# Kernel optimization log

Measured on AMD Instinct MI355X. Metric: run time of the kernel, lower is better.

The kernel has to match this reference:

```python
import jax, jax.numpy as jnp
import numpy as np

WS = 800      # window size
HEADS = 3
DH = 24       # dim_head
LOWRANK_W = 30
NEG_SLOPE = 0.01  # LeakyReLU default
LN_EPS = 1e-5


def _layernorm(x, g, b):
    m = jnp.mean(x, axis=-1, keepdims=True)
    v = jnp.var(x, axis=-1, keepdims=True)
    return (x - m) * jax.lax.rsqrt(v + LN_EPS) * g + b


def setup_inputs() -> dict:
    key = jax.random.key(0)
    ks = jax.random.split(key, 20)
    B, CIN, H, W = 2, 5, 160, 160
    D = 48
    INNER = HEADS * DH  # 72
    f32 = jnp.float32

    def n(k, shape, s=0.05):
        return jax.random.normal(k, shape, f32) * s

    return {
        "x": jax.random.normal(ks[0], (B, CIN, H, W), f32),
        # Embedding: Conv2d(5, 48, 3, pad=1) + PReLU
        "conv_w": n(ks[1], (D, CIN, 3, 3), 0.1),
        "conv_b": jnp.zeros((D,), f32),
        "prelu_a": jnp.array(0.25, f32),
        # attention PreNorm
        "ln1_g": jnp.ones((D,), f32),
        "ln1_b": jnp.zeros((D,), f32),
        # to_qkv: Linear(48, 216, bias=False)
        "w_qkv": n(ks[2], (3 * INNER, D)),
        # Linformer low-rank params E,F: [heads, dim_head, w]
        "E_mat": jax.random.normal(ks[3], (HEADS, DH, LOWRANK_W), f32),
        "F_mat": jax.random.normal(ks[4], (HEADS, DH, LOWRANK_W), f32),
        # lin1/lin2: Linear(w, dim_head)
        "w_e": n(ks[5], (DH, LOWRANK_W)),
        "b_e": jnp.zeros((DH,), f32),
        "w_f": n(ks[6], (DH, LOWRANK_W)),
        "b_f": jnp.zeros((DH,), f32),
        # to_out: Linear(72, 48)
        "w_out": n(ks[7], (D, INNER)),
        "b_out": jnp.zeros((D,), f32),
        # FF PreNorm + MLP (dim=48, hidden=48)
        "ln2_g": jnp.ones((D,), f32),
        "ln2_b": jnp.zeros((D,), f32),
        "ff_w1": n(ks[8], (D, D)),
        "ff_b1": jnp.zeros((D,), f32),
        "ff_w2": n(ks[9], (D, D)),
        "ff_b2": jnp.zeros((D,), f32),
        # final lin1: Linear(48, 96)
        "w_fin": n(ks[10], (2 * D, D)),
        "b_fin": jnp.zeros((2 * D,), f32),
    }


def reference(x, conv_w, conv_b, prelu_a, ln1_g, ln1_b, w_qkv, E_mat, F_mat,
              w_e, b_e, w_f, b_f, w_out, b_out, ln2_g, ln2_b,
              ff_w1, ff_b1, ff_w2, ff_b2, w_fin, b_fin):
    B, _, H, W = x.shape
    # Embedding: conv3x3 same + PReLU
    E = jax.lax.conv_general_dilated(
        x, conv_w, (1, 1), ((1, 1), (1, 1)),
        dimension_numbers=("NCHW", "OIHW", "NCHW")) + conv_b[None, :, None, None]
    E = jnp.maximum(E, 0) + prelu_a * jnp.minimum(E, 0)
    D = E.shape[1]
    seq = E.reshape(B, D, H * W).transpose(0, 2, 1)  # [B, N, D]
    N = seq.shape[1]
    nw = N // WS

    # --- Residual(PreNorm(LinformerAttention_wind1)) ---
    xn = _layernorm(seq, ln1_g, ln1_b)
    xw = xn.reshape(B, nw, WS, D)                         # windows
    qkv = jnp.einsum("bwnc,oc->bwno", xw, w_qkv)          # [B,nw,WS,216]
    qkv = qkv.reshape(B, nw, WS, HEADS, 3 * DH).transpose(0, 1, 3, 2, 4)
    q, k, v = jnp.split(qkv, 3, axis=-1)                  # each [B,nw,h,WS,DH]
    # einsum 'b h n d, h d d -> b h n d' == scale by diagonal of lin(E/F)
    e_diag = jnp.einsum("hdw,dw->hd", E_mat, w_e) + b_e   # [h, DH]
    f_diag = jnp.einsum("hdw,dw->hd", F_mat, w_f) + b_f
    k = k * e_diag[None, None, :, None, :]
    v = v * f_diag[None, None, :, None, :]
    scale = DH ** -0.5
    dots = jnp.einsum("bwhid,bwhjd->bwhij", q, k) * scale  # [B,nw,h,WS,WS]
    attn = jax.nn.softmax(dots, axis=-1)
    ow = jnp.einsum("bwhij,bwhjd->bwhid", attn, v)
    ow = ow.transpose(0, 1, 3, 2, 4).reshape(B, N, HEADS * DH)
    att = jnp.einsum("bnf,of->bno", ow, w_out) + b_out
    seq = seq + att

    # --- Residual(PreNorm(FeedForward)) ---
    yn = _layernorm(seq, ln2_g, ln2_b)
    h = jnp.einsum("bnc,oc->bno", yn, ff_w1) + ff_b1
    h = jnp.where(h >= 0, h, NEG_SLOPE * h)
    h = jnp.einsum("bno,co->bnc", h, ff_w2) + ff_b2
    att1 = seq + h                                        # [B, N, D]

    hp = att1.transpose(0, 2, 1).reshape(B, D, H, W)
    Highpass1 = E * hp + E
    lin = jnp.einsum("bnc,oc->bno", att1, w_fin) + b_fin  # [B, N, 2D]
    return (Highpass1, lin)
```

## Files before the change

kernel.cpp:

```cpp
#include <hip/hip_runtime.h>
#include <hip/hip_bf16.h>

#define B_    2
#define CIN_  5
#define H_    160
#define W_    160
#define N_    25600
#define D_    48
#define NW_   32
#define WS_   800
#define HEADS_ 3
#define DH_   24
#define INNER_ 72
#define NWH_  192

typedef __bf16 bf16x8 __attribute__((ext_vector_type(8)));
typedef float  f32x4  __attribute__((ext_vector_type(4)));

#define MFMA(a,b,c) __builtin_amdgcn_mfma_f32_16x16x32_bf16((a),(b),(c),0,0,0)

__device__ __forceinline__ float fast_exp2(float x) {
#if __has_builtin(__builtin_amdgcn_exp2f)
    return __builtin_amdgcn_exp2f(x);
#else
    return exp2f(x);
#endif
}

__device__ __forceinline__ unsigned pack_bf16(float lo, float hi) {
    __bf16 l = (__bf16)lo, h = (__bf16)hi;
    unsigned short ul = __builtin_bit_cast(unsigned short, l);
    unsigned short uh = __builtin_bit_cast(unsigned short, h);
    return ((unsigned)uh << 16) | (unsigned)ul;
}

__global__ __launch_bounds__(256) void k_wprep(const float* __restrict__ wqkv,
                                               const float* __restrict__ w_out,
                                               const float* __restrict__ fw1,
                                               const float* __restrict__ fw2,
                                               const float* __restrict__ wfin,
                                               const float* __restrict__ cw,
                                               const float* __restrict__ Em,
                                               const float* __restrict__ Fm,
                                               const float* __restrict__ we,
                                               const float* __restrict__ be,
                                               const float* __restrict__ wf,
                                               const float* __restrict__ bf,
                                               float* __restrict__ diag,
                                               __bf16* __restrict__ wqB,
                                               __bf16* __restrict__ woB,
                                               __bf16* __restrict__ f1B,
                                               __bf16* __restrict__ f2B,
                                               __bf16* __restrict__ wfB,
                                               __bf16* __restrict__ wcB) {
    if (blockIdx.x == 0 && threadIdx.x < 72) {
        int tt = threadIdx.x;
        int h = tt / 24, d = tt % 24;
        float se = be[d], sf = bf[d];
        for (int w = 0; w < 30; ++w) {
            se += Em[(h*24+d)*30 + w] * we[d*30 + w];
            sf += Fm[(h*24+d)*30 + w] * wf[d*30 + w];
        }
        diag[tt]      = se;
        diag[72 + tt] = sf;
    }
    int t = blockIdx.x*256 + threadIdx.x, stride = gridDim.x*256;
    for (int i = t; i < 288*64; i += stride) {
        int grow = i>>6, c = i&63;
        int gg = grow>>5, q = grow&31, tt = q>>4, sp = q&15, d = tt*16+sp;
        int part = gg/3, head = gg%3;
        wqB[i] = (d<24 && c<48) ? (__bf16)wqkv[(head*72 + part*24 + d)*48 + c] : (__bf16)0.f;
    }
    for (int i = t; i < 48*96;  i += stride) {
        int o = i/96, p = i%96;
        int h = p>>5, q = p&31, j = q&1, sp = q>>1, d = j*16+sp;
        woB[i] = (d<24) ? (__bf16)w_out[o*72 + h*24 + d] : (__bf16)0.f;
    }
    for (int i = t; i < 48*64;  i += stride) { int o=i>>6, c=i&63; f1B[i] = (c<48)? (__bf16)fw1[o*48+c] : (__bf16)0.f; }
    for (int i = t; i < 48*64;  i += stride) { int o=i>>6, c=i&63; f2B[i] = (c<48)? (__bf16)fw2[o*48+c] : (__bf16)0.f; }
    for (int i = t; i < 96*64;  i += stride) { int o=i>>6, c=i&63; wfB[i] = (c<48)? (__bf16)wfin[o*48+c] : (__bf16)0.f; }
    for (int i = t; i < 48*64;  i += stride) { int o=i>>6, c=i&63; wcB[i] = (c<45)? (__bf16)cw[o*45+c] : (__bf16)0.f; }
}

__global__ __launch_bounds__(128) void k_cqkv(const float* __restrict__ x,
                                              const __bf16* __restrict__ wcB,
                                              const float* __restrict__ cb,
                                              const float* __restrict__ pa,
                                              const __bf16* __restrict__ wqB,
                                              const float* __restrict__ g1,
                                              const float* __restrict__ b1,
                                              const float* __restrict__ diag,
                                              float* __restrict__ seqT,
                                              __bf16* __restrict__ Qbf,
                                              __bf16* __restrict__ Kbf,
                                              __bf16* __restrict__ Vt) {
    __shared__ float Lx[CIN_][4][W_];
    __shared__ __bf16 xfer[2][2048];
    int t = threadIdx.x;
    int blk = blockIdx.x;
    int b = blk / 400;
    int n0 = (blk % 400) * 64;
    int y0 = n0 / W_;

    for (int i = t; i < CIN_*4*W_; i += 128) {
        int ic = i / (4*W_), rem = i % (4*W_), yy = rem / W_, col = rem % W_;
        int yr = y0 - 1 + yy;
        float v = 0.f;
        if (yr >= 0 && yr < H_)
            v = x[((size_t)(b*CIN_ + ic)*H_ + yr)*W_ + col];
        Lx[ic][yy][col] = v;
    }
    __syncthreads();

    int wv = t >> 6, lane = t & 63, g = lane>>4, s = lane&15;
    int grow0 = blk*64 + wv*32;

    bf16x8 ac[2][2];
    #pragma unroll
    for (int m = 0; m < 2; ++m) {
        int row = wv*32 + m*16 + s;
        int n  = n0 + row;
        int y  = n / W_, xx = n % W_;
        int dy = y - y0;
        #pragma unroll
        for (int kc = 0; kc < 2; ++kc) {
            int kbase = kc*32 + g*8;
            #pragma unroll
            for (int j = 0; j < 8; ++j) {
                int k = kbase + j;
                int ic = k / 9, rem = k % 9, ky = rem / 3, kx = rem % 3;
                int xc = xx + kx - 1;
                float v = 0.f;
                if ((kc == 0 || k < 45) && xc >= 0 && xc < W_)
                    v = Lx[ic][dy + ky][xc];
                ac[m][kc][j] = (__bf16)v;
            }
        }
    }

    const bf16x8* WC4 = (const bf16x8*)wcB;
    float a = pa[0];
    float cbv[3];
    #pragma unroll
    for (int n = 0; n < 3; ++n) cbv[n] = cb[n*16+s];

    float xr[2][3][4];
    #pragma unroll
    for (int n = 0; n < 3; ++n) {
        bf16x8 wb0 = WC4[(n*16+s)*8 + g];
        bf16x8 wb1 = WC4[(n*16+s)*8 + 4 + g];
        #pragma unroll
        for (int m = 0; m < 2; ++m) {
            f32x4 c = {0.f,0.f,0.f,0.f};
            c = MFMA(ac[m][0], wb0, c);
            c = MFMA(ac[m][1], wb1, c);
            #pragma unroll
            for (int r = 0; r < 4; ++r) {
                float vv = c[r] + cbv[n];
                vv = vv >= 0.f ? vv : a * vv;
                xr[m][n][r] = vv;
            }
        }
    }
    #pragma unroll
    for (int m = 0; m < 2; ++m)
      #pragma unroll
      for (int n = 0; n < 3; ++n)
        #pragma unroll
        for (int r = 0; r < 4; ++r)
          seqT[(size_t)(grow0 + m*16 + g*4 + r)*48 + n*16 + s] = xr[m][n][r];

    char* xb = (char*)&xfer[wv][0];
    int nrem = grow0 % N_;
    int w = nrem / WS_, i0 = nrem % WS_;
    size_t headbase = (size_t)((b*NW_ + w)*HEADS_);

    float g1v[3], b1v[3];
    #pragma unroll
    for (int n = 0; n < 3; ++n) { g1v[n] = g1[n*16+s]; b1v[n] = b1[n*16+s]; }

    #pragma unroll
    for (int m = 0; m < 2; ++m)
      #pragma unroll
      for (int r = 0; r < 4; ++r) {
        float sm = xr[m][0][r] + xr[m][1][r] + xr[m][2][r];
        float sq = xr[m][0][r]*xr[m][0][r] + xr[m][1][r]*xr[m][1][r] + xr[m][2][r]*xr[m][2][r];
        #pragma unroll
        for (int msk = 1; msk < 16; msk <<= 1) { sm += __shfl_xor(sm, msk); sq += __shfl_xor(sq, msk); }
        float mean = sm * (1.f/48.f);
        float var  = sq * (1.f/48.f) - mean*mean;
        float rs   = rsqrtf(var + 1e-5f);
        int row = m*16 + g*4 + r;
        int sw  = ((g*4+r)&7) << 4;
        #pragma unroll
        for (int n = 0; n < 3; ++n) {
            float yn = (xr[m][n][r] - mean) * rs * g1v[n] + b1v[n];
            *(__bf16*)(xb + ((row*128 + (n*16+s)*2) ^ sw)) = (__bf16)yn;
        }
        *(__bf16*)(xb + ((row*128 + (48+s)*2) ^ sw)) = (__bf16)0.f;
      }

    bf16x8 af[2][2];
    #pragma unroll
    for (int m = 0; m < 2; ++m)
      #pragma unroll
      for (int kc = 0; kc < 2; ++kc)
        af[m][kc] = *(const bf16x8*)(xb + (((m*16+s)*128 + kc*64 + g*16) ^ ((s&7)<<4)));

    const bf16x8* WQ4 = (const bf16x8*)wqB;
    const float SCALE = 0.2944889919f;

    float dke[3], dko[3], dve[3], dvo[3];
    #pragma unroll
    for (int h = 0; h < 3; ++h) {
        dke[h] = diag[h*24 + s];
        dko[h] = (s < 8) ? diag[h*24 + 16 + s] : 0.f;
        dve[h] = diag[72 + h*24 + s];
        dvo[h] = (s < 8) ? diag[72 + h*24 + 16 + s] : 0.f;
    }

    unsigned* Qd = (unsigned*)Qbf;
    unsigned* Kd = (unsigned*)Kbf;

    #pragma unroll
    for (int gg = 0; gg < 9; ++gg) {
        int part = gg / 3, head = gg % 3;
        bf16x8 we0 = WQ4[(gg*32 +      s)*8 +     g];
        bf16x8 we1 = WQ4[(gg*32 +      s)*8 + 4 + g];
        bf16x8 wo0 = WQ4[(gg*32 + 16 + s)*8 +     g];
        bf16x8 wo1 = WQ4[(gg*32 + 16 + s)*8 + 4 + g];
        f32x4 ce[2], co[2];
        #pragma unroll
        for (int m = 0; m < 2; ++m) {
            f32x4 c = {0.f,0.f,0.f,0.f};
            c = MFMA(af[m][0], we0, c); c = MFMA(af[m][1], we1, c);
            ce[m] = c;
            f32x4 d = {0.f,0.f,0.f,0.f};
            d = MFMA(af[m][0], wo0, d); d = MFMA(af[m][1], wo1, d);
            co[m] = d;
        }
        size_t rbase = (headbase + head)*WS_ + i0;
        if (part == 0) {
            #pragma unroll
            for (int m = 0; m < 2; ++m)
              #pragma unroll
              for (int r = 0; r < 4; ++r)
                Qd[(rbase + m*16 + g*4 + r)*16 + s] =
                    pack_bf16(ce[m][r]*SCALE, co[m][r]*SCALE);
        } else if (part == 1) {
            #pragma unroll
            for (int m = 0; m < 2; ++m)
              #pragma unroll
              for (int r = 0; r < 4; ++r) {
                int p5 = 16*(g&1) + 8*m + 4*(g>>1) + r;
                Kd[(rbase + p5)*16 + s] =
                    pack_bf16(ce[m][r]*dke[head], co[m][r]*dko[head]);
              }
        } else {
            size_t vbase = (headbase + head)*((size_t)32*WS_) + i0;
            #pragma unroll
            for (int m = 0; m < 2; ++m)
              #pragma unroll
              for (int r = 0; r < 4; ++r) {
                int row = m*16 + g*4 + r;
                Vt[vbase + (size_t)s*WS_ + row] = (__bf16)(ce[m][r]*dve[head]);
                if (s < 8)
                    Vt[vbase + (size_t)(16+s)*WS_ + row] = (__bf16)(co[m][r]*dvo[head]);
              }
        }
    }
    unsigned* Vd = (unsigned*)Vt;
    #pragma unroll
    for (int it = 0; it < 6; ++it) {
        int idx = it*64 + lane;
        int h = idx >> 7, rem = idx & 127;
        int dd = 24 + (rem >> 4), cp = rem & 15;
        size_t ubase = (((headbase + h)*((size_t)32*WS_) + (size_t)dd*WS_ + i0) >> 1);
        Vd[ubase + cp] = (dd == 24) ? 0x3F803F80u : 0u;
    }
}

__global__ __launch_bounds__(256, 4) void k_attn(const __bf16* __restrict__ Qbf,
                                                 const __bf16* __restrict__ Kbf,
                                                 const __bf16* __restrict__ Vt,
                                                 __bf16* __restrict__ OW) {
    __shared__ float red[2][5][2][4][64];
    int t = threadIdx.x;
    int wv = t >> 6, lane = t & 63;
    int g = lane >> 4, s = lane & 15;
    int half = wv & 1, tsk = wv >> 1;
    int blk = blockIdx.x;
    int v = (blk & 7) * 120 + (blk >> 3);
    int task = v * 2 + tsk;
    int wh = task / 10, qt = task % 10;
    int q0 = qt * 80;

    const bf16x8* Qp = (const bf16x8*)(Qbf + ((size_t)wh*WS_ + q0)*32);
    const bf16x8* Kp = (const bf16x8*)(Kbf + (size_t)wh*WS_*32);
    const bf16x8* Vp = (const bf16x8*)(Vt  + (size_t)wh*32*WS_);

    bf16x8 qb[5];
    #pragma unroll
    for (int i = 0; i < 5; ++i) qb[i] = Qp[(i*16 + s)*4 + g];

    f32x4 o[5][2];
    #pragma unroll
    for (int i = 0; i < 5; ++i) {
        o[i][0] = (f32x4){0.f,0.f,0.f,0.f};
        o[i][1] = (f32x4){0.f,0.f,0.f,0.f};
    }

    int c0 = half ? 12 : 0;
    int c1 = half ? 25 : 12;

    bf16x8 ka0 = Kp[(c0*32 + s)*4 + g];
    bf16x8 ka1 = Kp[(c0*32 + 16 + s)*4 + g];
    bf16x8 vb0 = Vp[s*100 + c0*4 + g];
    bf16x8 vb1 = Vp[(16+s)*100 + c0*4 + g];

    for (int c = c0; c < c1; ++c) {
        int cn = (c + 1 < c1) ? c + 1 : c0;
        bf16x8 nk0 = Kp[(cn*32 + s)*4 + g];
        bf16x8 nk1 = Kp[(cn*32 + 16 + s)*4 + g];
        bf16x8 nv0 = Vp[s*100 + cn*4 + g];
        bf16x8 nv1 = Vp[(16+s)*100 + cn*4 + g];

        #pragma unroll
        for (int i = 0; i < 5; ++i) {
            f32x4 s0 = {0.f,0.f,0.f,0.f}, s1 = {0.f,0.f,0.f,0.f};
            s0 = MFMA(ka0, qb[i], s0);
            s1 = MFMA(ka1, qb[i], s1);
            bf16x8 pa;
            #pragma unroll
            for (int r = 0; r < 4; ++r) {
                pa[r]     = (__bf16)fast_exp2(s0[r]);
                pa[r + 4] = (__bf16)fast_exp2(s1[r]);
            }
            o[i][0] = MFMA(pa, vb0, o[i][0]);
            o[i][1] = MFMA(pa, vb1, o[i][1]);
        }
        ka0 = nk0; ka1 = nk1; vb0 = nv0; vb1 = nv1;
    }

    if (half) {
        #pragma unroll
        for (int i = 0; i < 5; ++i)
          #pragma unroll
          for (int j = 0; j < 2; ++j)
            #pragma unroll
            for (int r = 0; r < 4; ++r)
              red[tsk][i][j][r][lane] = o[i][j][r];
    }
    __syncthreads();
    if (!half) {
        #pragma unroll
        for (int i = 0; i < 5; ++i)
          #pragma unroll
          for (int j = 0; j < 2; ++j)
            #pragma unroll
            for (int r = 0; r < 4; ++r)
              o[i][j][r] += red[tsk][i][j][r][lane];

        int bw = wh / 3, h = wh % 3;
        int b = bw >> 5, w = bw & 31;
        unsigned* OWd = (unsigned*)OW;
        #pragma unroll
        for (int i = 0; i < 5; ++i) {
            #pragma unroll
            for (int r = 0; r < 4; ++r) {
                float den = __shfl(o[i][1][r], (lane & 48) + 8);
                float inv = 1.f / den;
                int n = w*WS_ + q0 + i*16 + g*4 + r;
                OWd[(size_t)(b*N_ + n)*48 + h*16 + s] =
                    pack_bf16(o[i][0][r]*inv, o[i][1][r]*inv);
            }
        }
    }
}

__global__ __launch_bounds__(256) void k_tail(const float* __restrict__ seqT,
                                              const __bf16* __restrict__ OW,
                                              const __bf16* __restrict__ woB,
                                              const float* __restrict__ b_out,
                                              const float* __restrict__ g2,
                                              const float* __restrict__ b2,
                                              const __bf16* __restrict__ f1B,
                                              const float* __restrict__ fb1,
                                              const __bf16* __restrict__ f2B,
                                              const float* __restrict__ fb2,
                                              const __bf16* __restrict__ wfB,
                                              const float* __restrict__ bfin,
                                              float* __restrict__ out1,
                                              float* __restrict__ out2) {
    __shared__ __bf16 xfer[4][2048];
    __shared__ float hp[4][32][49];
    int t = threadIdx.x, wv = t>>6, lane = t&63, g = lane>>4, s = lane&15;
    int row0 = (blockIdx.x*4 + wv) * 32;
    char* xb = (char*)&xfer[wv][0];

    int b = row0 / N_;
    int nbase = row0 % N_;

    const bf16x8* OW4 = (const bf16x8*)OW;
    const bf16x8* WO4 = (const bf16x8*)woB;
    const bf16x8* F14 = (const bf16x8*)f1B;
    const bf16x8* F24 = (const bf16x8*)f2B;
    const bf16x8* WF4 = (const bf16x8*)wfB;

    bf16x8 aow[2][3];
    #pragma unroll
    for (int m = 0; m < 2; ++m)
      #pragma unroll
      for (int kc = 0; kc < 3; ++kc)
        aow[m][kc] = OW4[(size_t)(row0 + m*16 + s)*12 + kc*4 + g];

    f32x4 s2[2][3];
    #pragma unroll
    for (int n = 0; n < 3; ++n) {
        bf16x8 wb0 = WO4[(n*16+s)*12 + g];
        bf16x8 wb1 = WO4[(n*16+s)*12 + 4 + g];
        bf16x8 wb2 = WO4[(n*16+s)*12 + 8 + g];
        #pragma unroll
        for (int m = 0; m < 2; ++m) {
            f32x4 c = {0.f,0.f,0.f,0.f};
            c = MFMA(aow[m][0], wb0, c);
            c = MFMA(aow[m][1], wb1, c);
            c = MFMA(aow[m][2], wb2, c);
            s2[m][n] = c;
        }
    }
    float bov[3], g2v[3], b2v[3], f1bv[3], f2bv[3];
    #pragma unroll
    for (int n = 0; n < 3; ++n) {
        bov[n] = b_out[n*16+s]; g2v[n] = g2[n*16+s]; b2v[n] = b2[n*16+s];
        f1bv[n] = fb1[n*16+s];  f2bv[n] = fb2[n*16+s];
    }
    float sv[2][3][4];
    #pragma unroll
    for (int m = 0; m < 2; ++m)
      #pragma unroll
      for (int n = 0; n < 3; ++n)
        #pragma unroll
        for (int r = 0; r < 4; ++r) {
          sv[m][n][r] = seqT[(size_t)(row0 + m*16 + g*4 + r)*48 + n*16 + s];
          s2[m][n][r] += sv[m][n][r] + bov[n];
        }

    #pragma unroll
    for (int m = 0; m < 2; ++m)
      #pragma unroll
      for (int r = 0; r < 4; ++r) {
        float sm = s2[m][0][r] + s2[m][1][r] + s2[m][2][r];
        float sq = s2[m][0][r]*s2[m][0][r] + s2[m][1][r]*s2[m][1][r] + s2[m][2][r]*s2[m][2][r];
        #pragma unroll
        for (int msk = 1; msk < 16; msk <<= 1) { sm += __shfl_xor(sm, msk); sq += __shfl_xor(sq, msk); }
        float mean = sm * (1.f/48.f);
        float var  = sq * (1.f/48.f) - mean*mean;
        float rs   = rsqrtf(var + 1e-5f);
        int row = m*16 + g*4 + r;
        int sw  = ((g*4+r)&7) << 4;
        #pragma unroll
        for (int n = 0; n < 3; ++n) {
            float yn = (s2[m][n][r] - mean) * rs * g2v[n] + b2v[n];
            *(__bf16*)(xb + ((row*128 + (n*16+s)*2) ^ sw)) = (__bf16)yn;
        }
        *(__bf16*)(xb + ((row*128 + (48+s)*2) ^ sw)) = (__bf16)0.f;
      }

    bf16x8 af[2][2];
    f32x4 hh[2][3];

    #pragma unroll
    for (int m = 0; m < 2; ++m)
      #pragma unroll
      for (int kc = 0; kc < 2; ++kc)
        af[m][kc] = *(const bf16x8*)(xb + (((m*16+s)*128 + kc*64 + g*16) ^ ((s&7)<<4)));
    #pragma unroll
    for (int n = 0; n < 3; ++n) {
        bf16x8 wb0 = F14[(n*16+s)*8 + g];
        bf16x8 wb1 = F14[(n*16+s)*8 + 4 + g];
        #pragma unroll
        for (int m = 0; m < 2; ++m) {
            f32x4 c = {0.f,0.f,0.f,0.f};
            c = MFMA(af[m][0], wb0, c);
            c = MFMA(af[m][1], wb1, c);
            hh[m][n] = c;
        }
    }
    #pragma unroll
    for (int m = 0; m < 2; ++m)
      #pragma unroll
      for (int r = 0; r < 4; ++r) {
        int row = m*16 + g*4 + r;
        int sw  = ((g*4+r)&7) << 4;
        #pragma unroll
        for (int n = 0; n < 3; ++n) {
            float v = hh[m][n][r] + f1bv[n];
            v = v >= 0.f ? v : 0.01f*v;
            *(__bf16*)(xb + ((row*128 + (n*16+s)*2) ^ sw)) = (__bf16)v;
        }
        *(__bf16*)(xb + ((row*128 + (48+s)*2) ^ sw)) = (__bf16)0.f;
      }

    #pragma unroll
    for (int m = 0; m < 2; ++m)
      #pragma unroll
      for (int kc = 0; kc < 2; ++kc)
        af[m][kc] = *(const bf16x8*)(xb + (((m*16+s)*128 + kc*64 + g*16) ^ ((s&7)<<4)));
    #pragma unroll
    for (int n = 0; n < 3; ++n) {
        bf16x8 wb0 = F24[(n*16+s)*8 + g];
        bf16x8 wb1 = F24[(n*16+s)*8 + 4 + g];
        #pragma unroll
        for (int m = 0; m < 2; ++m) {
            f32x4 c = {0.f,0.f,0.f,0.f};
            c = MFMA(af[m][0], wb0, c);
            c = MFMA(af[m][1], wb1, c);
            hh[m][n] = c;
        }
    }
    #pragma unroll
    for (int m = 0; m < 2; ++m)
      #pragma unroll
      for (int r = 0; r < 4; ++r) {
        int row = m*16 + g*4 + r;
        int sw  = ((g*4+r)&7) << 4;
        #pragma unroll
        for (int n = 0; n < 3; ++n) {
            float a1v = s2[m][n][r] + hh[m][n][r] + f2bv[n];
            hp[wv][row][n*16+s] = sv[m][n][r] * (1.f + a1v);
            *(__bf16*)(xb + ((row*128 + (n*16+s)*2) ^ sw)) = (__bf16)a1v;
        }
        *(__bf16*)(xb + ((row*128 + (48+s)*2) ^ sw)) = (__bf16)0.f;
      }

    #pragma unroll
    for (int it = 0; it < 6; ++it) {
        int flat = it*256 + lane*4;
        int ch = flat >> 5, row = flat & 31;
        float4 v = { hp[wv][row][ch], hp[wv][row+1][ch],
                     hp[wv][row+2][ch], hp[wv][row+3][ch] };
        *(float4*)&out1[((size_t)b*D_ + ch)*N_ + nbase + row] = v;
    }

    #pragma unroll
    for (int m = 0; m < 2; ++m)
      #pragma unroll
      for (int kc = 0; kc < 2; ++kc)
        af[m][kc] = *(const bf16x8*)(xb + (((m*16+s)*128 + kc*64 + g*16) ^ ((s&7)<<4)));
    #pragma unroll
    for (int n = 0; n < 6; ++n) {
        bf16x8 wb0 = WF4[(n*16+s)*8 + g];
        bf16x8 wb1 = WF4[(n*16+s)*8 + 4 + g];
        float bfv = bfin[n*16+s];
        #pragma unroll
        for (int m = 0; m < 2; ++m) {
            f32x4 c = {0.f,0.f,0.f,0.f};
            c = MFMA(af[m][0], wb0, c);
            c = MFMA(af[m][1], wb1, c);
            #pragma unroll
            for (int r = 0; r < 4; ++r)
                out2[(size_t)(row0 + m*16 + g*4 + r)*96 + n*16 + s] = c[r] + bfv;
        }
    }
}

extern "C" void kernel_launch(void* const* d_in, const int* in_sizes, int n_in,
                              void* d_out, int out_size, void* d_ws, size_t ws_size,
                              hipStream_t stream) {
    const float* x      = (const float*)d_in[0];
    const float* conv_w = (const float*)d_in[1];
    const float* conv_b = (const float*)d_in[2];
    const float* prelu_a= (const float*)d_in[3];
    const float* ln1_g  = (const float*)d_in[4];
    const float* ln1_b  = (const float*)d_in[5];
    const float* w_qkv  = (const float*)d_in[6];
    const float* E_mat  = (const float*)d_in[7];
    const float* F_mat  = (const float*)d_in[8];
    const float* w_e    = (const float*)d_in[9];
    const float* b_e    = (const float*)d_in[10];
    const float* w_f    = (const float*)d_in[11];
    const float* b_f    = (const float*)d_in[12];
    const float* w_out  = (const float*)d_in[13];
    const float* b_out  = (const float*)d_in[14];
    const float* ln2_g  = (const float*)d_in[15];
    const float* ln2_b  = (const float*)d_in[16];
    const float* ff_w1  = (const float*)d_in[17];
    const float* ff_b1  = (const float*)d_in[18];
    const float* ff_w2  = (const float*)d_in[19];
    const float* ff_b2  = (const float*)d_in[20];
    const float* w_fin  = (const float*)d_in[21];
    const float* b_fin  = (const float*)d_in[22];

    float* ws = (float*)d_ws;
    float*  seqT = ws;
    float*  diag = seqT + (size_t)B_*N_*D_;
    __bf16* Qbf  = (__bf16*)(diag + 144);
    __bf16* Kbf  = Qbf + (size_t)NWH_*WS_*32;
    __bf16* Vt   = Kbf + (size_t)NWH_*WS_*32;
    __bf16* OW   = Vt + (size_t)NWH_*32*WS_;
    __bf16* wqB  = OW + (size_t)B_*N_*96;
    __bf16* woB  = wqB + 288*64;
    __bf16* f1B  = woB + 48*96;
    __bf16* f2B  = f1B + 48*64;
    __bf16* wfB  = f2B + 48*64;
    __bf16* wcB  = wfB + 96*64;

    float* out1 = (float*)d_out;
    float* out2 = out1 + (size_t)B_*D_*N_;

    k_wprep<<<32, 256, 0, stream>>>(w_qkv, w_out, ff_w1, ff_w2, w_fin, conv_w,
                                    E_mat, F_mat, w_e, b_e, w_f, b_f, diag,
                                    wqB, woB, f1B, f2B, wfB, wcB);
    k_cqkv<<<800, 128, 0, stream>>>(x, wcB, conv_b, prelu_a,
                                    wqB, ln1_g, ln1_b, diag, seqT, Qbf, Kbf, Vt);
    k_attn<<<960, 256, 0, stream>>>(Qbf, Kbf, Vt, OW);
    k_tail<<<400, 256, 0, stream>>>(seqT, OW, woB, b_out, ln2_g, ln2_b,
                                    f1B, ff_b1, f2B, ff_b2, wfB, b_fin,
                                    out1, out2);
}
```

Measured before the change: 82.25 us.

## Split conv+QKV kernel work across four waves per block

The fused conv/LayerNorm/QKV kernel moves from 128 to 256 threads per block. Each of the four waves now computes the conv and LayerNorm for 16 rows and writes them into a block-shared LDS tile. After a barrier, the QKV projection groups are split between wave pairs (5 and 4 groups), and the V padding writes go to one half. This aims to raise parallelism and latency hiding in a small-grid kernel, at the cost of an extra block barrier and an uneven split of QKV work.

```diff
diff --git a/kernel.cpp b/kernel.cpp
--- a/kernel.cpp
+++ b/kernel.cpp
@@ -82,7 +82,7 @@
     for (int i = t; i < 48*64;  i += stride) { int o=i>>6, c=i&63; wcB[i] = (c<45)? (__bf16)cw[o*45+c] : (__bf16)0.f; }
 }
 
-__global__ __launch_bounds__(128) void k_cqkv(const float* __restrict__ x,
+__global__ __launch_bounds__(256) void k_cqkv(const float* __restrict__ x,
                                               const __bf16* __restrict__ wcB,
                                               const float* __restrict__ cb,
                                               const float* __restrict__ pa,
@@ -95,14 +95,14 @@
                                               __bf16* __restrict__ Kbf,
                                               __bf16* __restrict__ Vt) {
     __shared__ float Lx[CIN_][4][W_];
-    __shared__ __bf16 xfer[2][2048];
+    __shared__ __bf16 xfer[64*64];
     int t = threadIdx.x;
     int blk = blockIdx.x;
     int b = blk / 400;
     int n0 = (blk % 400) * 64;
     int y0 = n0 / W_;
 
-    for (int i = t; i < CIN_*4*W_; i += 128) {
+    for (int i = t; i < CIN_*4*W_; i += 256) {
         int ic = i / (4*W_), rem = i % (4*W_), yy = rem / W_, col = rem % W_;
         int yr = y0 - 1 + yy;
         float v = 0.f;
@@ -113,99 +113,95 @@
     __syncthreads();
 
     int wv = t >> 6, lane = t & 63, g = lane>>4, s = lane&15;
-    int grow0 = blk*64 + wv*32;
-
-    bf16x8 ac[2][2];
-    #pragma unroll
-    for (int m = 0; m < 2; ++m) {
-        int row = wv*32 + m*16 + s;
-        int n  = n0 + row;
-        int y  = n / W_, xx = n % W_;
-        int dy = y - y0;
-        #pragma unroll
-        for (int kc = 0; kc < 2; ++kc) {
-            int kbase = kc*32 + g*8;
-            #pragma unroll
-            for (int j = 0; j < 8; ++j) {
-                int k = kbase + j;
-                int ic = k / 9, rem = k % 9, ky = rem / 3, kx = rem % 3;
-                int xc = xx + kx - 1;
-                float v = 0.f;
-                if ((kc == 0 || k < 45) && xc >= 0 && xc < W_)
-                    v = Lx[ic][dy + ky][xc];
-                ac[m][kc][j] = (__bf16)v;
+    char* xb = (char*)xfer;
+
+    {
+        int rloc0 = wv * 16;
+        bf16x8 ac[2];
+        {
+            int row = rloc0 + s;
+            int n  = n0 + row;
+            int y  = n / W_, xx = n % W_;
+            int dy = y - y0;
+            #pragma unroll
+            for (int kc = 0; kc < 2; ++kc) {
+                int kbase = kc*32 + g*8;
+                #pragma unroll
+                for (int j = 0; j < 8; ++j) {
+                    int k = kbase + j;
+                    int ic = k / 9, rem = k % 9, ky = rem / 3, kx = rem % 3;
+                    int xc = xx + kx - 1;
+                    float v = 0.f;
+                    if ((kc == 0 || k < 45) && xc >= 0 && xc < W_)
+                        v = Lx[ic][dy + ky][xc];
+                    ac[kc][j] = (__bf16)v;
+                }
             }
         }
-    }
-
-    const bf16x8* WC4 = (const bf16x8*)wcB;
-    float a = pa[0];
-    float cbv[3];
-    #pragma unroll
-    for (int n = 0; n < 3; ++n) cbv[n] = cb[n*16+s];
-
-    float xr[2][3][4];
-    #pragma unroll
-    for (int n = 0; n < 3; ++n) {
-        bf16x8 wb0 = WC4[(n*16+s)*8 + g];
-        bf16x8 wb1 = WC4[(n*16+s)*8 + 4 + g];
-        #pragma unroll
-        for (int m = 0; m < 2; ++m) {
+        const bf16x8* WC4 = (const bf16x8*)wcB;
+        float a = pa[0];
+        float cbv[3], g1v[3], b1v[3];
+        #pragma unroll
+        for (int n = 0; n < 3; ++n) {
+            cbv[n] = cb[n*16+s]; g1v[n] = g1[n*16+s]; b1v[n] = b1[n*16+s];
+        }
+        float xr[3][4];
+        #pragma unroll
+        for (int n = 0; n < 3; ++n) {
+            bf16x8 wb0 = WC4[(n*16+s)*8 + g];
+            bf16x8 wb1 = WC4[(n*16+s)*8 + 4 + g];
             f32x4 c = {0.f,0.f,0.f,0.f};
-            c = MFMA(ac[m][0], wb0, c);
-            c = MFMA(ac[m][1], wb1, c);
+            c = MFMA(ac[0], wb0, c);
+            c = MFMA(ac[1], wb1, c);
             #pragma unroll
             for (int r = 0; r < 4; ++r) {
                 float vv = c[r] + cbv[n];
                 vv = vv >= 0.f ? vv : a * vv;
-                xr[m][n][r] = vv;
+                xr[n][r] = vv;
             }
         }
-    }
-    #pragma unroll
-    for (int m = 0; m < 2; ++m)
-      #pragma unroll
-      for (int n = 0; n < 3; ++n)
-        #pragma unroll
-        for (int r = 0; r < 4; ++r)
-          seqT[(size_t)(grow0 + m*16 + g*4 + r)*48 + n*16 + s] = xr[m][n][r];
-
-    char* xb = (char*)&xfer[wv][0];
-    int nrem = grow0 % N_;
+        int grow0 = blk*64 + rloc0;
+        #pragma unroll
+        for (int n = 0; n < 3; ++n)
+          #pragma unroll
+          for (int r = 0; r < 4; ++r)
+            seqT[(size_t)(grow0 + g*4 + r)*48 + n*16 + s] = xr[n][r];
+
+        #pragma unroll
+        for (int r = 0; r < 4; ++r) {
+            float sm = xr[0][r] + xr[1][r] + xr[2][r];
+            float sq = xr[0][r]*xr[0][r] + xr[1][r]*xr[1][r] + xr[2][r]*xr[2][r];
+            #pragma unroll
+            for (int msk = 1; msk < 16; msk <<= 1) { sm += __shfl_xor(sm, msk); sq += __shfl_xor(sq, msk); }
+            float mean = sm * (1.f/48.f);
+            float var  = sq * (1.f/48.f) - mean*mean;
+            float rs   = rsqrtf(var + 1e-5f);
+            int row = rloc0 + g*4 + r;
+            int sw  = ((g*4+r)&7) << 4;
+            #pragma unroll
+            for (int n = 0; n < 3; ++n) {
+                float yn = (xr[n][r] - mean) * rs * g1v[n] + b1v[n];
+                *(__bf16*)(xb + ((row*128 + (n*16+s)*2) ^ sw)) = (__bf16)yn;
+            }
+            *(__bf16*)(xb + ((row*128 + (48+s)*2) ^ sw)) = (__bf16)0.f;
+        }
+    }
+    __syncthreads();
+
+    int rh = wv & 1, gh = wv >> 1;
+    int growQ = blk*64 + rh*32;
+    int nrem = growQ % N_;
     int w = nrem / WS_, i0 = nrem % WS_;
     size_t headbase = (size_t)((b*NW_ + w)*HEADS_);
 
-    float g1v[3], b1v[3];
-    #pragma unroll
-    for (int n = 0; n < 3; ++n) { g1v[n] = g1[n*16+s]; b1v[n] = b1[n*16+s]; }
-
-    #pragma unroll
-    for (int m = 0; m < 2; ++m)
-      #pragma unroll
-      for (int r = 0; r < 4; ++r) {
-        float sm = xr[m][0][r] + xr[m][1][r] + xr[m][2][r];
-        float sq = xr[m][0][r]*xr[m][0][r] + xr[m][1][r]*xr[m][1][r] + xr[m][2][r]*xr[m][2][r];
-        #pragma unroll
-        for (int msk = 1; msk < 16; msk <<= 1) { sm += __shfl_xor(sm, msk); sq += __shfl_xor(sq, msk); }
-        float mean = sm * (1.f/48.f);
-        float var  = sq * (1.f/48.f) - mean*mean;
-        float rs   = rsqrtf(var + 1e-5f);
-        int row = m*16 + g*4 + r;
-        int sw  = ((g*4+r)&7) << 4;
-        #pragma unroll
-        for (int n = 0; n < 3; ++n) {
-            float yn = (xr[m][n][r] - mean) * rs * g1v[n] + b1v[n];
-            *(__bf16*)(xb + ((row*128 + (n*16+s)*2) ^ sw)) = (__bf16)yn;
-        }
-        *(__bf16*)(xb + ((row*128 + (48+s)*2) ^ sw)) = (__bf16)0.f;
+    bf16x8 af[2][2];
+    #pragma unroll
+    for (int m = 0; m < 2; ++m)
+      #pragma unroll
+      for (int kc = 0; kc < 2; ++kc) {
+        int row = rh*32 + m*16 + s;
+        af[m][kc] = *(const bf16x8*)(xb + ((row*128 + kc*64 + g*16) ^ ((s&7)<<4)));
       }
-
-    bf16x8 af[2][2];
-    #pragma unroll
-    for (int m = 0; m < 2; ++m)
-      #pragma unroll
-      for (int kc = 0; kc < 2; ++kc)
-        af[m][kc] = *(const bf16x8*)(xb + (((m*16+s)*128 + kc*64 + g*16) ^ ((s&7)<<4)));
 
     const bf16x8* WQ4 = (const bf16x8*)wqB;
     const float SCALE = 0.2944889919f;
@@ -222,8 +218,8 @@
     unsigned* Qd = (unsigned*)Qbf;
     unsigned* Kd = (unsigned*)Kbf;
 
-    #pragma unroll
-    for (int gg = 0; gg < 9; ++gg) {
+    int gg0 = gh ? 5 : 0, gg1 = gh ? 9 : 5;
+    for (int gg = gg0; gg < gg1; ++gg) {
         int part = gg / 3, head = gg % 3;
         bf16x8 we0 = WQ4[(gg*32 +      s)*8 +     g];
         bf16x8 we1 = WQ4[(gg*32 +      s)*8 + 4 + g];
@@ -269,14 +265,16 @@
               }
         }
     }
-    unsigned* Vd = (unsigned*)Vt;
-    #pragma unroll
-    for (int it = 0; it < 6; ++it) {
-        int idx = it*64 + lane;
-        int h = idx >> 7, rem = idx & 127;
-        int dd = 24 + (rem >> 4), cp = rem & 15;
-        size_t ubase = (((headbase + h)*((size_t)32*WS_) + (size_t)dd*WS_ + i0) >> 1);
-        Vd[ubase + cp] = (dd == 24) ? 0x3F803F80u : 0u;
+    if (gh == 1) {
+        unsigned* Vd = (unsigned*)Vt;
+        #pragma unroll
+        for (int it = 0; it < 6; ++it) {
+            int idx = it*64 + lane;
+            int h = idx >> 7, rem = idx & 127;
+            int dd = 24 + (rem >> 4), cp = rem & 15;
+            size_t ubase = (((headbase + h)*((size_t)32*WS_) + (size_t)dd*WS_ + i0) >> 1);
+            Vd[ubase + cp] = (dd == 24) ? 0x3F803F80u : 0u;
+        }
     }
 }
 
@@ -612,7 +610,7 @@
     k_wprep<<<32, 256, 0, stream>>>(w_qkv, w_out, ff_w1, ff_w2, w_fin, conv_w,
                                     E_mat, F_mat, w_e, b_e, w_f, b_f, diag,
                                     wqB, woB, f1B, f2B, wfB, wcB);
-    k_cqkv<<<800, 128, 0, stream>>>(x, wcB, conv_b, prelu_a,
+    k_cqkv<<<800, 256, 0, stream>>>(x, wcB, conv_b, prelu_a,
                                     wqB, ln1_g, ln1_b, diag, seqT, Qbf, Kbf, Vt);
     k_attn<<<960, 256, 0, stream>>>(Qbf, Kbf, Vt, OW);
     k_tail<<<400, 256, 0, stream>>>(seqT, OW, woB, b_out, ln2_g, ln2_b,
```

Measured after the change: 79.72 us. -3.1%, faster.
